# Kernel optimization log

Hardware: AMD Instinct MI355X
Metric: run time of the kernel (lower is better)

## Reference

```python
import jax, jax.numpy as jnp
import numpy as np

N = 50000      # nodes
E = 640000     # edges (before self loops)
IN = 128       # in_channels
H = 4          # heads (layer 1)
C = 64         # hidden_channels per head
OUT = 64       # out_channels
SLOPE = 0.2    # PyG GATConv default negative_slope


def setup_inputs() -> dict:
    key = jax.random.key(0)
    ks = jax.random.split(key, 12)
    x = jax.random.normal(ks[0], (N, IN), dtype=jnp.float32)
    edge_src = jax.random.randint(ks[1], (E,), 0, N, dtype=jnp.int32)
    edge_dst = jax.random.randint(ks[2], (E,), 0, N, dtype=jnp.int32)
    # Layer 1 params: Linear IN -> H*C, attention vectors a_src/a_dst [H, C], bias [H*C]
    W1 = jax.random.normal(ks[3], (IN, H * C), dtype=jnp.float32) / np.sqrt(IN)
    att_src1 = jax.random.normal(ks[4], (H, C), dtype=jnp.float32) / np.sqrt(C)
    att_dst1 = jax.random.normal(ks[5], (H, C), dtype=jnp.float32) / np.sqrt(C)
    b1 = jnp.zeros((H * C,), dtype=jnp.float32)
    # Layer 2 params: Linear H*C -> OUT, 1 head
    W2 = jax.random.normal(ks[6], (H * C, OUT), dtype=jnp.float32) / np.sqrt(H * C)
    att_src2 = jax.random.normal(ks[7], (1, OUT), dtype=jnp.float32) / np.sqrt(OUT)
    att_dst2 = jax.random.normal(ks[8], (1, OUT), dtype=jnp.float32) / np.sqrt(OUT)
    b2 = jnp.zeros((OUT,), dtype=jnp.float32)
    return {"x": x, "W1": W1, "att_src1": att_src1, "att_dst1": att_dst1, "b1": b1,
            "W2": W2, "att_src2": att_src2, "att_dst2": att_dst2, "b2": b2,
            "edge_src": edge_src, "edge_dst": edge_dst}


def gat_conv(x, src, dst, W, a_src, a_dst, b, heads, ch):
    """PyG GATConv (concat=True): gather -> LeakyReLU attention -> per-dst softmax -> scatter-add."""
    n = x.shape[0]
    h = (x @ W).reshape(n, heads, ch)                  # [N, H, C]
    al_s = jnp.sum(h * a_src, axis=-1)                 # [N, H] node-level src attention term
    al_d = jnp.sum(h * a_dst, axis=-1)                 # [N, H]
    e = jax.nn.leaky_relu(al_s[src] + al_d[dst], SLOPE)  # [E, H] edge scores
    m = jax.ops.segment_max(e, dst, num_segments=n)    # stable per-dst softmax
    ex = jnp.exp(e - m[dst])
    den = jax.ops.segment_sum(ex, dst, num_segments=n)
    alpha = ex / den[dst]                              # [E, H]
    msg = h[src] * alpha[:, :, None]                   # [E, H, C]
    out = jax.ops.segment_sum(msg, dst, num_segments=n)  # [N, H, C]
    return out.reshape(n, heads * ch) + b


def reference(x, W1, att_src1, att_dst1, b1, W2, att_src2, att_dst2, b2, edge_src, edge_dst):
    # PyG GATConv default add_self_loops=True
    loops = jnp.arange(N, dtype=edge_src.dtype)
    src = jnp.concatenate([edge_src, loops])
    dst = jnp.concatenate([edge_dst, loops])
    h = gat_conv(x, src, dst, W1, att_src1, att_dst1, b1, H, C)
    h = jax.nn.elu(h)                                  # F.elu; dropout p=0 -> no-op
    out = gat_conv(h, src, dst, W2, att_src2, att_dst2, b2, 1, OUT)
    return out
```

## Files before the change

### kernel.cpp

```cpp
#include <hip/hip_runtime.h>
#include <hip/hip_bf16.h>
#include <cstdint>
#include <cstddef>

#define N_NODES 50000
#define N_EDGES 640000
#define ET (N_EDGES + N_NODES)
#define IN_CH 128
#define H1 4
#define HC1 256
#define OUT_CH 64
#define SLOPE 0.2f
#define SCAN_NBLK ((N_NODES + 255) / 256)
#define XW (N_NODES * IN_CH / 8)
#define W1N (IN_CH * HC1)
#define W2N (HC1 * OUT_CH)
#define CONVB ((XW + W1N + W2N + 255) / 256)
#define EDGEB ((ET + 255) / 256)
#define MT ((N_NODES + 63) / 64)
#define PADB SCAN_NBLK
#define DUMMY N_NODES

typedef __attribute__((ext_vector_type(8))) short short8;
typedef __attribute__((ext_vector_type(4))) float floatx4;

__device__ __forceinline__ float bf2f(unsigned short u) {
    return __uint_as_float(((unsigned)u) << 16);
}
__device__ __forceinline__ unsigned short f2bf(float f) {
    unsigned u = __float_as_uint(f);
    unsigned r = 0x7fffu + ((u >> 16) & 1u);
    return (unsigned short)((u + r) >> 16);
}
__device__ __forceinline__ float ldf(const void* p, size_t i, bool f32) {
    return f32 ? ((const float*)p)[i] : bf2f(((const unsigned short*)p)[i]);
}

__global__ __launch_bounds__(256) void init_all(
    const unsigned short* __restrict__ x, unsigned* __restrict__ flag,
    int* __restrict__ counts, int* __restrict__ state,
    unsigned short* __restrict__ h16, unsigned short* __restrict__ h2,
    float* __restrict__ als1, float* __restrict__ als2)
{
    int b = blockIdx.x;
    if (b < SCAN_NBLK) {
        int i = b * 256 + threadIdx.x;
        if (i < N_NODES) counts[i] = 0;
    } else {
        int t = threadIdx.x;
        if (t < 64) {
            int bad = 0;
            #pragma unroll
            for (int r = 0; r < 4; ++r) {
                float v = bf2f(x[r * 64 + t]);
                if (!(v == v) || fabsf(v) > 1e4f) bad = 1;
            }
            unsigned long long m = __ballot(bad != 0);
            if (t == 0) *flag = (m != 0ull) ? 1u : 0u;
        } else if (t == 64) {
            state[0] = 0; state[1] = 0;
        } else if (t >= 128 && t < 192) {
            uint2 z; z.x = 0u; z.y = 0u;
            *((uint2*)(h16 + (size_t)DUMMY * HC1) + (t - 128)) = z;
        } else if (t >= 192 && t < 224) {
            ((unsigned*)(h2 + (size_t)DUMMY * OUT_CH))[t - 192] = 0u;
        } else if (t >= 224 && t < 228) {
            als1[(size_t)DUMMY * H1 + (t - 224)] = -1e30f;
        } else if (t == 228) {
            als2[DUMMY] = -1e30f;
        }
    }
}

__global__ __launch_bounds__(256) void conv_count(
    const void* __restrict__ x, const void* __restrict__ W1,
    const void* __restrict__ W2, const unsigned* __restrict__ flag,
    unsigned short* __restrict__ x16,
    unsigned short* __restrict__ Wt1, unsigned short* __restrict__ Wt2,
    const int* __restrict__ edst, int* __restrict__ counts,
    int* __restrict__ epos)
{
    int b = blockIdx.x;
    if (b < CONVB) {
        int i = b * 256 + threadIdx.x;
        const bool f32 = (*flag != 0);
        if (i < XW) {
            size_t off = (size_t)i * 8;
            uint4 st;
            if (f32) {
                const float* xp = (const float*)x + off;
                float4 a = *(const float4*)xp;
                float4 c = *(const float4*)(xp + 4);
                st.x = (unsigned)f2bf(a.x) | ((unsigned)f2bf(a.y) << 16);
                st.y = (unsigned)f2bf(a.z) | ((unsigned)f2bf(a.w) << 16);
                st.z = (unsigned)f2bf(c.x) | ((unsigned)f2bf(c.y) << 16);
                st.w = (unsigned)f2bf(c.z) | ((unsigned)f2bf(c.w) << 16);
            } else {
                st = *(const uint4*)((const unsigned short*)x + off);
            }
            *(uint4*)(x16 + off) = st;
        } else if (i < XW + W1N) {
            int j = i - XW;
            int n = j / IN_CH, k = j % IN_CH;
            Wt1[j] = f2bf(ldf(W1, (size_t)k * HC1 + n, f32));
        } else if (i < XW + W1N + W2N) {
            int j = i - XW - W1N;
            int n = j / HC1, k = j % HC1;
            Wt2[j] = f2bf(ldf(W2, (size_t)k * OUT_CH + n, f32));
        }
    } else {
        int i = (b - CONVB) * 256 + threadIdx.x;
        if (i < ET) {
            int d = (i < N_EDGES) ? edst[i] : (i - N_EDGES);
            epos[i] = atomicAdd(&counts[d], 1);
        }
    }
}

__global__ __launch_bounds__(256) void scan_onepass(
    const int* __restrict__ counts, int* __restrict__ rowptr,
    int* __restrict__ bsum, int* __restrict__ boff, int* __restrict__ state)
{
    __shared__ int s[256];
    const int t = threadIdx.x, b = blockIdx.x;
    const int i = b * 256 + t;
    int v = (i < N_NODES) ? ((counts[i] + 7) & ~7) : 0;
    s[t] = v;
    __syncthreads();
    #pragma unroll
    for (int off = 1; off < 256; off <<= 1) {
        int u = (t >= off) ? s[t - off] : 0;
        __syncthreads();
        s[t] += u;
        __syncthreads();
    }
    const int incl = s[t];
    if (t == 255) {
        __hip_atomic_store(&bsum[b], incl, __ATOMIC_RELAXED, __HIP_MEMORY_SCOPE_AGENT);
        __hip_atomic_fetch_add(&state[0], 1, __ATOMIC_ACQ_REL, __HIP_MEMORY_SCOPE_AGENT);
    }
    if (b == 0) {
        if (t == 0) {
            while (__hip_atomic_load(&state[0], __ATOMIC_ACQUIRE, __HIP_MEMORY_SCOPE_AGENT) < SCAN_NBLK)
                __builtin_amdgcn_s_sleep(8);
        }
        __syncthreads();
        int w = (t < SCAN_NBLK)
              ? __hip_atomic_load(&bsum[t], __ATOMIC_RELAXED, __HIP_MEMORY_SCOPE_AGENT) : 0;
        s[t] = w;
        __syncthreads();
        #pragma unroll
        for (int off = 1; off < 256; off <<= 1) {
            int u = (t >= off) ? s[t - off] : 0;
            __syncthreads();
            s[t] += u;
            __syncthreads();
        }
        if (t < SCAN_NBLK)
            __hip_atomic_store(&boff[t], s[t] - w, __ATOMIC_RELAXED, __HIP_MEMORY_SCOPE_AGENT);
        __syncthreads();
        if (t == 0)
            __hip_atomic_store(&state[1], 1, __ATOMIC_RELEASE, __HIP_MEMORY_SCOPE_AGENT);
    }
    if (t == 0) {
        while (__hip_atomic_load(&state[1], __ATOMIC_ACQUIRE, __HIP_MEMORY_SCOPE_AGENT) == 0)
            __builtin_amdgcn_s_sleep(8);
    }
    __syncthreads();
    int off0 = __hip_atomic_load(&boff[b], __ATOMIC_RELAXED, __HIP_MEMORY_SCOPE_AGENT);
    if (i < N_NODES)
        rowptr[i] = off0 + incl - v;
    if (i == N_NODES - 1) rowptr[N_NODES] = off0 + incl;
}

template <int KK, int NSUB>
__device__ __forceinline__ void gemm_body(
    const unsigned short* __restrict__ A, const unsigned short* __restrict__ Bt,
    const void* __restrict__ avs, const void* __restrict__ avd,
    const unsigned* __restrict__ flag, unsigned short* __restrict__ C,
    float* __restrict__ als, float* __restrict__ ald,
    int M, int N, int bx, int by)
{
    const int tid = threadIdx.x;
    const int m0 = by * 64, n0 = bx * (NSUB * 16);
    const int w = tid >> 6, lane = tid & 63;
    const int ln = lane & 15, quad = lane >> 4;
    const int m_frag = m0 + w * 16 + ln;
    floatx4 acc[NSUB];
    #pragma unroll
    for (int sub = 0; sub < NSUB; ++sub)
        acc[sub] = (floatx4){0.f, 0.f, 0.f, 0.f};

    #pragma unroll 2
    for (int ks = 0; ks < KK / 32; ++ks) {
        const int kbase = ks * 32 + quad * 8;
        short8 a;
        if (m_frag < M) {
            a = *(const short8*)(A + (size_t)m_frag * KK + kbase);
        } else {
            #pragma unroll
            for (int j = 0; j < 8; ++j) a[j] = 0;
        }
        #pragma unroll
        for (int sub = 0; sub < NSUB; ++sub) {
            short8 b = *(const short8*)(Bt + (size_t)(n0 + sub * 16 + ln) * KK + kbase);
            acc[sub] = __builtin_amdgcn_mfma_f32_16x16x32_bf16(a, b, acc[sub], 0, 0, 0);
        }
    }

    #pragma unroll
    for (int sub = 0; sub < NSUB; ++sub) {
        #pragma unroll
        for (int r = 0; r < 4; ++r) {
            int m = m0 + w * 16 + quad * 4 + r;
            if (m < M)
                C[(size_t)m * N + n0 + sub * 16 + ln] = f2bf(acc[sub][r]);
        }
    }

    const bool f32in = (*flag != 0);
    float as[NSUB], av[NSUB];
    #pragma unroll
    for (int sub = 0; sub < NSUB; ++sub) {
        as[sub] = ldf(avs, n0 + sub * 16 + ln, f32in);
        av[sub] = ldf(avd, n0 + sub * 16 + ln, f32in);
    }
    const int Hh = N >> 6;
    #pragma unroll
    for (int hb = 0; hb < NSUB / 4; ++hb) {
        #pragma unroll
        for (int r = 0; r < 4; ++r) {
            float ps = 0.f, pd = 0.f;
            #pragma unroll
            for (int k = 0; k < 4; ++k) {
                ps += acc[hb * 4 + k][r] * as[hb * 4 + k];
                pd += acc[hb * 4 + k][r] * av[hb * 4 + k];
            }
            #pragma unroll
            for (int off = 1; off < 16; off <<= 1) {
                ps += __shfl_xor(ps, off, 64);
                pd += __shfl_xor(pd, off, 64);
            }
            int m = m0 + w * 16 + quad * 4 + r;
            if (ln == 0 && m < M) {
                als[(size_t)m * Hh + bx * (NSUB / 4) + hb] = ps;
                ald[(size_t)m * Hh + bx * (NSUB / 4) + hb] = pd;
            }
        }
    }
}

__global__ __launch_bounds__(256) void gemm1_fill(
    const unsigned short* __restrict__ x16, const unsigned short* __restrict__ Wt1,
    const void* __restrict__ as1, const void* __restrict__ ad1,
    const unsigned* __restrict__ flag, unsigned short* __restrict__ h16,
    float* __restrict__ als, float* __restrict__ ald,
    const int* __restrict__ esrc, const int* __restrict__ edst,
    const int* __restrict__ rowptr, const int* __restrict__ epos,
    const int* __restrict__ counts, int* __restrict__ ecsr)
{
    int b = blockIdx.x;
    if (b < MT) {
        gemm_body<IN_CH, 16>(x16, Wt1, as1, ad1, flag, h16, als, ald,
                             N_NODES, HC1, 0, b);
    } else if (b < MT + EDGEB) {
        int i = (b - MT) * 256 + threadIdx.x;
        if (i < ET) {
            int s = (i < N_EDGES) ? esrc[i] : (i - N_EDGES);
            int d = (i < N_EDGES) ? edst[i] : (i - N_EDGES);
            ecsr[rowptr[d] + epos[i]] = s;
        }
    } else {
        int i = (b - MT - EDGEB) * 256 + threadIdx.x;
        if (i < N_NODES) {
            int c = counts[i];
            int lo = rowptr[i] + c, hi = rowptr[i + 1];
            for (int j = lo; j < hi; ++j) ecsr[j] = DUMMY;
        }
    }
}

__global__ __launch_bounds__(256) void gemm2(
    const unsigned short* __restrict__ xo16, const unsigned short* __restrict__ Wt2,
    const void* __restrict__ as2, const void* __restrict__ ad2,
    const unsigned* __restrict__ flag, unsigned short* __restrict__ h2,
    float* __restrict__ als, float* __restrict__ ald)
{
    gemm_body<HC1, 4>(xo16, Wt2, as2, ad2, flag, h2, als, ald,
                      N_NODES, OUT_CH, 0, blockIdx.x);
}

__global__ __launch_bounds__(256) void agg_node1(
    const int* __restrict__ rowptr, const int* __restrict__ ecsr,
    const unsigned short* __restrict__ h, const float* __restrict__ als,
    const float* __restrict__ ald, const void* __restrict__ bias,
    const unsigned* __restrict__ flag, unsigned short* __restrict__ out)
{
    int wave = (blockIdx.x * blockDim.x + threadIdx.x) >> 6;
    int lane = threadIdx.x & 63;
    if (wave >= N_NODES) return;
    const int d = wave;
    const int hg = lane >> 4;
    const int c0 = (lane & 15) << 2;
    const int hoff = hg * 64 + c0;
    const int lo = rowptr[d], hi = rowptr[d + 1];
    const float ad = ald[d * H1 + hg];

    float acc0 = 0.f, acc1 = 0.f, acc2 = 0.f, acc3 = 0.f, den = 0.f;

    int4 iA = *(const int4*)(ecsr + lo);
    int4 iB = *(const int4*)(ecsr + lo + 4);
    for (int e = lo; e < hi; e += 8) {
        const int4 cA = iA, cB = iB;
        const int en = (e + 8 < hi) ? (e + 8) : lo;
        iA = *(const int4*)(ecsr + en);
        iB = *(const int4*)(ecsr + en + 4);

        uint2 q0 = *(const uint2*)(h + (size_t)cA.x * HC1 + hoff);
        uint2 q1 = *(const uint2*)(h + (size_t)cA.y * HC1 + hoff);
        uint2 q2 = *(const uint2*)(h + (size_t)cA.z * HC1 + hoff);
        uint2 q3 = *(const uint2*)(h + (size_t)cA.w * HC1 + hoff);
        uint2 q4 = *(const uint2*)(h + (size_t)cB.x * HC1 + hoff);
        uint2 q5 = *(const uint2*)(h + (size_t)cB.y * HC1 + hoff);
        uint2 q6 = *(const uint2*)(h + (size_t)cB.z * HC1 + hoff);
        uint2 q7 = *(const uint2*)(h + (size_t)cB.w * HC1 + hoff);
        float t0 = als[cA.x * H1 + hg] + ad;
        float t1 = als[cA.y * H1 + hg] + ad;
        float t2 = als[cA.z * H1 + hg] + ad;
        float t3 = als[cA.w * H1 + hg] + ad;
        float t4 = als[cB.x * H1 + hg] + ad;
        float t5 = als[cB.y * H1 + hg] + ad;
        float t6 = als[cB.z * H1 + hg] + ad;
        float t7 = als[cB.w * H1 + hg] + ad;
        float p0 = __expf(fmaxf(t0, SLOPE * t0));
        float p1 = __expf(fmaxf(t1, SLOPE * t1));
        float p2 = __expf(fmaxf(t2, SLOPE * t2));
        float p3 = __expf(fmaxf(t3, SLOPE * t3));
        float p4 = __expf(fmaxf(t4, SLOPE * t4));
        float p5 = __expf(fmaxf(t5, SLOPE * t5));
        float p6 = __expf(fmaxf(t6, SLOPE * t6));
        float p7 = __expf(fmaxf(t7, SLOPE * t7));
        den += ((p0 + p1) + (p2 + p3)) + ((p4 + p5) + (p6 + p7));
        acc0 += p0 * __uint_as_float(q0.x << 16)         + p1 * __uint_as_float(q1.x << 16)
              + p2 * __uint_as_float(q2.x << 16)         + p3 * __uint_as_float(q3.x << 16)
              + p4 * __uint_as_float(q4.x << 16)         + p5 * __uint_as_float(q5.x << 16)
              + p6 * __uint_as_float(q6.x << 16)         + p7 * __uint_as_float(q7.x << 16);
        acc1 += p0 * __uint_as_float(q0.x & 0xffff0000u) + p1 * __uint_as_float(q1.x & 0xffff0000u)
              + p2 * __uint_as_float(q2.x & 0xffff0000u) + p3 * __uint_as_float(q3.x & 0xffff0000u)
              + p4 * __uint_as_float(q4.x & 0xffff0000u) + p5 * __uint_as_float(q5.x & 0xffff0000u)
              + p6 * __uint_as_float(q6.x & 0xffff0000u) + p7 * __uint_as_float(q7.x & 0xffff0000u);
        acc2 += p0 * __uint_as_float(q0.y << 16)         + p1 * __uint_as_float(q1.y << 16)
              + p2 * __uint_as_float(q2.y << 16)         + p3 * __uint_as_float(q3.y << 16)
              + p4 * __uint_as_float(q4.y << 16)         + p5 * __uint_as_float(q5.y << 16)
              + p6 * __uint_as_float(q6.y << 16)         + p7 * __uint_as_float(q7.y << 16);
        acc3 += p0 * __uint_as_float(q0.y & 0xffff0000u) + p1 * __uint_as_float(q1.y & 0xffff0000u)
              + p2 * __uint_as_float(q2.y & 0xffff0000u) + p3 * __uint_as_float(q3.y & 0xffff0000u)
              + p4 * __uint_as_float(q4.y & 0xffff0000u) + p5 * __uint_as_float(q5.y & 0xffff0000u)
              + p6 * __uint_as_float(q6.y & 0xffff0000u) + p7 * __uint_as_float(q7.y & 0xffff0000u);
    }

    const bool f32in = (*flag != 0);
    const float inv = 1.f / den;
    float v0 = acc0 * inv + ldf(bias, hoff + 0, f32in);
    float v1 = acc1 * inv + ldf(bias, hoff + 1, f32in);
    float v2 = acc2 * inv + ldf(bias, hoff + 2, f32in);
    float v3 = acc3 * inv + ldf(bias, hoff + 3, f32in);
    v0 = (v0 > 0.f) ? v0 : (__expf(v0) - 1.f);
    v1 = (v1 > 0.f) ? v1 : (__expf(v1) - 1.f);
    v2 = (v2 > 0.f) ? v2 : (__expf(v2) - 1.f);
    v3 = (v3 > 0.f) ? v3 : (__expf(v3) - 1.f);
    uint2 st;
    st.x = (unsigned)f2bf(v0) | ((unsigned)f2bf(v1) << 16);
    st.y = (unsigned)f2bf(v2) | ((unsigned)f2bf(v3) << 16);
    *(uint2*)(out + (size_t)d * HC1 + hoff) = st;
}

__global__ __launch_bounds__(256) void agg_node2(
    const int* __restrict__ rowptr, const int* __restrict__ ecsr,
    const unsigned short* __restrict__ h, const float* __restrict__ als,
    const float* __restrict__ ald, const void* __restrict__ bias,
    const unsigned* __restrict__ flag, float* __restrict__ out)
{
    int wave = (blockIdx.x * blockDim.x + threadIdx.x) >> 6;
    int lane = threadIdx.x & 63;
    if (wave >= N_NODES) return;
    const int d = wave;
    const int eg = lane >> 3;
    const int c0 = (lane & 7) << 3;
    const int lo = rowptr[d], hi = rowptr[d + 1];
    const float ad = ald[d];

    float acc[8];
    #pragma unroll
    for (int j = 0; j < 8; ++j) acc[j] = 0.f;
    float den = 0.f;

    int sP = ecsr[lo + eg];
    for (int eb = lo; eb < hi; eb += 8) {
        const int s = sP;
        const int en = (eb + 8 < hi) ? (eb + 8) : lo;
        sP = ecsr[en + eg];
        uint4 q = *(const uint4*)(h + (size_t)s * OUT_CH + c0);
        float t = als[s] + ad;
        float p = __expf(fmaxf(t, SLOPE * t));
        den += p;
        acc[0] += p * __uint_as_float(q.x << 16);
        acc[1] += p * __uint_as_float(q.x & 0xffff0000u);
        acc[2] += p * __uint_as_float(q.y << 16);
        acc[3] += p * __uint_as_float(q.y & 0xffff0000u);
        acc[4] += p * __uint_as_float(q.z << 16);
        acc[5] += p * __uint_as_float(q.z & 0xffff0000u);
        acc[6] += p * __uint_as_float(q.w << 16);
        acc[7] += p * __uint_as_float(q.w & 0xffff0000u);
    }
    #pragma unroll
    for (int off = 8; off <= 32; off <<= 1) {
        den += __shfl_xor(den, off, 64);
        #pragma unroll
        for (int j = 0; j < 8; ++j) acc[j] += __shfl_xor(acc[j], off, 64);
    }
    if (lane < 8) {
        const bool f32in = (*flag != 0);
        const float inv = 1.f / den;
        float4 v0, v1;
        v0.x = acc[0] * inv + ldf(bias, c0 + 0, f32in);
        v0.y = acc[1] * inv + ldf(bias, c0 + 1, f32in);
        v0.z = acc[2] * inv + ldf(bias, c0 + 2, f32in);
        v0.w = acc[3] * inv + ldf(bias, c0 + 3, f32in);
        v1.x = acc[4] * inv + ldf(bias, c0 + 4, f32in);
        v1.y = acc[5] * inv + ldf(bias, c0 + 5, f32in);
        v1.z = acc[6] * inv + ldf(bias, c0 + 6, f32in);
        v1.w = acc[7] * inv + ldf(bias, c0 + 7, f32in);
        *(float4*)(out + (size_t)d * OUT_CH + c0) = v0;
        *(float4*)(out + (size_t)d * OUT_CH + c0 + 4) = v1;
    }
}

extern "C" void kernel_launch(void* const* d_in, const int* in_sizes, int n_in,
                              void* d_out, int out_size, void* d_ws, size_t ws_size,
                              hipStream_t stream)
{
    const void* x   = d_in[0];
    const void* W1  = d_in[1];
    const void* as1 = d_in[2];
    const void* ad1 = d_in[3];
    const void* b1  = d_in[4];
    const void* W2  = d_in[5];
    const void* as2 = d_in[6];
    const void* ad2 = d_in[7];
    const void* b2  = d_in[8];
    const int* esrc = (const int*)d_in[9];
    const int* edst = (const int*)d_in[10];
    float* out = (float*)d_out;

    char* base = (char*)d_ws;
    const size_t MB = 1024 * 1024;
    unsigned short* x16  = (unsigned short*)(base);
    unsigned short* h16  = (unsigned short*)(base + 13 * MB);
    unsigned short* xo16 = (unsigned short*)(base + 39 * MB);
    unsigned short* h2   = (unsigned short*)(base + 65 * MB);
    float* als1   = (float*)(base + 72 * MB);
    float* ald1   = (float*)(base + 73 * MB);
    float* als2   = (float*)(base + 74 * MB);
    float* ald2   = (float*)(base + 74 * MB + 512 * 1024);
    unsigned short* Wt1 = (unsigned short*)(base + 75 * MB);
    unsigned short* Wt2 = (unsigned short*)(base + 75 * MB + 128 * 1024);
    int* counts   = (int*)(base + 76 * MB);
    int* rowptr   = (int*)(base + 77 * MB);
    int* bsum     = (int*)(base + 78 * MB);
    int* boff     = bsum + 256;
    int* state    = boff + 256;
    unsigned* flag = (unsigned*)(base + 78 * MB + 8 * 1024);
    int* epos     = (int*)(base + 79 * MB);
    int* ecsr     = (int*)(base + 82 * MB);

    const int BLK = 256;
    const int node_wave_blocks = (N_NODES * 64 + BLK - 1) / BLK;

    init_all<<<SCAN_NBLK + 1, BLK, 0, stream>>>(
        (const unsigned short*)x, flag, counts, state, h16, h2, als1, als2);

    conv_count<<<CONVB + EDGEB, BLK, 0, stream>>>(
        x, W1, W2, flag, x16, Wt1, Wt2, edst, counts, epos);

    scan_onepass<<<SCAN_NBLK, BLK, 0, stream>>>(
        counts, rowptr, bsum, boff, state);

    gemm1_fill<<<MT + EDGEB + PADB, BLK, 0, stream>>>(
        x16, Wt1, as1, ad1, flag, h16, als1, ald1, esrc, edst, rowptr, epos,
        counts, ecsr);

    agg_node1<<<node_wave_blocks, BLK, 0, stream>>>(
        rowptr, ecsr, h16, als1, ald1, b1, flag, xo16);

    gemm2<<<MT, BLK, 0, stream>>>(xo16, Wt2, as2, ad2, flag, h2, als2, ald2);

    agg_node2<<<node_wave_blocks, BLK, 0, stream>>>(
        rowptr, ecsr, h2, als2, ald2, b2, flag, out);
}
```

Measured before the change: 291.8 us.

## Split GEMM1 into per-head column tiles and widen agg_node1 gather loads

GEMM1 now launches four blocks per 64-row tile, one per 64-column head slice (NSUB 4), instead of one block covering all 256 columns, giving more blocks and fewer accumulator registers per block. agg_node1 changes its lane mapping so each lane loads 8 bf16 channels (uint4) and the two half-waves process alternating edges, combined at the end with a shuffle. This trades the 8-edge unrolled prefetch for wider loads and fewer in-flight gathers per lane. agg_node2 drops its index prefetch and the gemm k-loop unroll pragma is removed.

```diff
diff --git a/kernel.cpp b/kernel.cpp
--- a/kernel.cpp
+++ b/kernel.cpp
@@ -18,6 +18,7 @@
 #define CONVB ((XW + W1N + W2N + 255) / 256)
 #define EDGEB ((ET + 255) / 256)
 #define MT ((N_NODES + 63) / 64)
+#define G1B (4 * MT)
 #define PADB SCAN_NBLK
 #define DUMMY N_NODES
 
@@ -35,6 +36,8 @@
 __device__ __forceinline__ float ldf(const void* p, size_t i, bool f32) {
     return f32 ? ((const float*)p)[i] : bf2f(((const unsigned short*)p)[i]);
 }
+#define BLO(u) __uint_as_float((u) << 16)
+#define BHI(u) __uint_as_float((u) & 0xffff0000u)
 
 __global__ __launch_bounds__(256) void init_all(
     const unsigned short* __restrict__ x, unsigned* __restrict__ flag,
@@ -191,7 +194,6 @@
     for (int sub = 0; sub < NSUB; ++sub)
         acc[sub] = (floatx4){0.f, 0.f, 0.f, 0.f};
 
-    #pragma unroll 2
     for (int ks = 0; ks < KK / 32; ++ks) {
         const int kbase = ks * 32 + quad * 8;
         short8 a;
@@ -260,18 +262,18 @@
     const int* __restrict__ counts, int* __restrict__ ecsr)
 {
     int b = blockIdx.x;
-    if (b < MT) {
-        gemm_body<IN_CH, 16>(x16, Wt1, as1, ad1, flag, h16, als, ald,
-                             N_NODES, HC1, 0, b);
-    } else if (b < MT + EDGEB) {
-        int i = (b - MT) * 256 + threadIdx.x;
+    if (b < G1B) {
+        gemm_body<IN_CH, 4>(x16, Wt1, as1, ad1, flag, h16, als, ald,
+                            N_NODES, HC1, b & 3, b >> 2);
+    } else if (b < G1B + EDGEB) {
+        int i = (b - G1B) * 256 + threadIdx.x;
         if (i < ET) {
             int s = (i < N_EDGES) ? esrc[i] : (i - N_EDGES);
             int d = (i < N_EDGES) ? edst[i] : (i - N_EDGES);
             ecsr[rowptr[d] + epos[i]] = s;
         }
     } else {
-        int i = (b - MT - EDGEB) * 256 + threadIdx.x;
+        int i = (b - G1B - EDGEB) * 256 + threadIdx.x;
         if (i < N_NODES) {
             int c = counts[i];
             int lo = rowptr[i] + c, hi = rowptr[i + 1];
@@ -300,79 +302,59 @@
     int lane = threadIdx.x & 63;
     if (wave >= N_NODES) return;
     const int d = wave;
-    const int hg = lane >> 4;
-    const int c0 = (lane & 15) << 2;
+    const int g  = lane >> 5;
+    const int hg = (lane >> 3) & 3;
+    const int c0 = (lane & 7) << 3;
     const int hoff = hg * 64 + c0;
     const int lo = rowptr[d], hi = rowptr[d + 1];
     const float ad = ald[d * H1 + hg];
 
-    float acc0 = 0.f, acc1 = 0.f, acc2 = 0.f, acc3 = 0.f, den = 0.f;
-
-    int4 iA = *(const int4*)(ecsr + lo);
-    int4 iB = *(const int4*)(ecsr + lo + 4);
-    for (int e = lo; e < hi; e += 8) {
-        const int4 cA = iA, cB = iB;
-        const int en = (e + 8 < hi) ? (e + 8) : lo;
-        iA = *(const int4*)(ecsr + en);
-        iB = *(const int4*)(ecsr + en + 4);
-
-        uint2 q0 = *(const uint2*)(h + (size_t)cA.x * HC1 + hoff);
-        uint2 q1 = *(const uint2*)(h + (size_t)cA.y * HC1 + hoff);
-        uint2 q2 = *(const uint2*)(h + (size_t)cA.z * HC1 + hoff);
-        uint2 q3 = *(const uint2*)(h + (size_t)cA.w * HC1 + hoff);
-        uint2 q4 = *(const uint2*)(h + (size_t)cB.x * HC1 + hoff);
-        uint2 q5 = *(const uint2*)(h + (size_t)cB.y * HC1 + hoff);
-        uint2 q6 = *(const uint2*)(h + (size_t)cB.z * HC1 + hoff);
-        uint2 q7 = *(const uint2*)(h + (size_t)cB.w * HC1 + hoff);
-        float t0 = als[cA.x * H1 + hg] + ad;
-        float t1 = als[cA.y * H1 + hg] + ad;
-        float t2 = als[cA.z * H1 + hg] + ad;
-        float t3 = als[cA.w * H1 + hg] + ad;
-        float t4 = als[cB.x * H1 + hg] + ad;
-        float t5 = als[cB.y * H1 + hg] + ad;
-        float t6 = als[cB.z * H1 + hg] + ad;
-        float t7 = als[cB.w * H1 + hg] + ad;
+    float acc[8];
+    #pragma unroll
+    for (int j = 0; j < 8; ++j) acc[j] = 0.f;
+    float den = 0.f;
+
+    for (int e = lo; e < hi; e += 4) {
+        int4 ix = *(const int4*)(ecsr + e);
+        int s0 = g ? ix.y : ix.x;
+        int s1 = g ? ix.w : ix.z;
+        uint4 qa = *(const uint4*)(h + (size_t)s0 * HC1 + hoff);
+        uint4 qb = *(const uint4*)(h + (size_t)s1 * HC1 + hoff);
+        float t0 = als[s0 * H1 + hg] + ad;
+        float t1 = als[s1 * H1 + hg] + ad;
         float p0 = __expf(fmaxf(t0, SLOPE * t0));
         float p1 = __expf(fmaxf(t1, SLOPE * t1));
-        float p2 = __expf(fmaxf(t2, SLOPE * t2));
-        float p3 = __expf(fmaxf(t3, SLOPE * t3));
-        float p4 = __expf(fmaxf(t4, SLOPE * t4));
-        float p5 = __expf(fmaxf(t5, SLOPE * t5));
-        float p6 = __expf(fmaxf(t6, SLOPE * t6));
-        float p7 = __expf(fmaxf(t7, SLOPE * t7));
-        den += ((p0 + p1) + (p2 + p3)) + ((p4 + p5) + (p6 + p7));
-        acc0 += p0 * __uint_as_float(q0.x << 16)         + p1 * __uint_as_float(q1.x << 16)
-              + p2 * __uint_as_float(q2.x << 16)         + p3 * __uint_as_float(q3.x << 16)
-              + p4 * __uint_as_float(q4.x << 16)         + p5 * __uint_as_float(q5.x << 16)
-              + p6 * __uint_as_float(q6.x << 16)         + p7 * __uint_as_float(q7.x << 16);
-        acc1 += p0 * __uint_as_float(q0.x & 0xffff0000u) + p1 * __uint_as_float(q1.x & 0xffff0000u)
-              + p2 * __uint_as_float(q2.x & 0xffff0000u) + p3 * __uint_as_float(q3.x & 0xffff0000u)
-              + p4 * __uint_as_float(q4.x & 0xffff0000u) + p5 * __uint_as_float(q5.x & 0xffff0000u)
-              + p6 * __uint_as_float(q6.x & 0xffff0000u) + p7 * __uint_as_float(q7.x & 0xffff0000u);
-        acc2 += p0 * __uint_as_float(q0.y << 16)         + p1 * __uint_as_float(q1.y << 16)
-              + p2 * __uint_as_float(q2.y << 16)         + p3 * __uint_as_float(q3.y << 16)
-              + p4 * __uint_as_float(q4.y << 16)         + p5 * __uint_as_float(q5.y << 16)
-              + p6 * __uint_as_float(q6.y << 16)         + p7 * __uint_as_float(q7.y << 16);
-        acc3 += p0 * __uint_as_float(q0.y & 0xffff0000u) + p1 * __uint_as_float(q1.y & 0xffff0000u)
-              + p2 * __uint_as_float(q2.y & 0xffff0000u) + p3 * __uint_as_float(q3.y & 0xffff0000u)
-              + p4 * __uint_as_float(q4.y & 0xffff0000u) + p5 * __uint_as_float(q5.y & 0xffff0000u)
-              + p6 * __uint_as_float(q6.y & 0xffff0000u) + p7 * __uint_as_float(q7.y & 0xffff0000u);
-    }
-
-    const bool f32in = (*flag != 0);
-    const float inv = 1.f / den;
-    float v0 = acc0 * inv + ldf(bias, hoff + 0, f32in);
-    float v1 = acc1 * inv + ldf(bias, hoff + 1, f32in);
-    float v2 = acc2 * inv + ldf(bias, hoff + 2, f32in);
-    float v3 = acc3 * inv + ldf(bias, hoff + 3, f32in);
-    v0 = (v0 > 0.f) ? v0 : (__expf(v0) - 1.f);
-    v1 = (v1 > 0.f) ? v1 : (__expf(v1) - 1.f);
-    v2 = (v2 > 0.f) ? v2 : (__expf(v2) - 1.f);
-    v3 = (v3 > 0.f) ? v3 : (__expf(v3) - 1.f);
-    uint2 st;
-    st.x = (unsigned)f2bf(v0) | ((unsigned)f2bf(v1) << 16);
-    st.y = (unsigned)f2bf(v2) | ((unsigned)f2bf(v3) << 16);
-    *(uint2*)(out + (size_t)d * HC1 + hoff) = st;
+        den += p0 + p1;
+        acc[0] += p0 * BLO(qa.x) + p1 * BLO(qb.x);
+        acc[1] += p0 * BHI(qa.x) + p1 * BHI(qb.x);
+        acc[2] += p0 * BLO(qa.y) + p1 * BLO(qb.y);
+        acc[3] += p0 * BHI(qa.y) + p1 * BHI(qb.y);
+        acc[4] += p0 * BLO(qa.z) + p1 * BLO(qb.z);
+        acc[5] += p0 * BHI(qa.z) + p1 * BHI(qb.z);
+        acc[6] += p0 * BLO(qa.w) + p1 * BLO(qb.w);
+        acc[7] += p0 * BHI(qa.w) + p1 * BHI(qb.w);
+    }
+
+    den += __shfl_xor(den, 32, 64);
+    #pragma unroll
+    for (int j = 0; j < 8; ++j) acc[j] += __shfl_xor(acc[j], 32, 64);
+
+    if (lane < 32) {
+        const bool f32in = (*flag != 0);
+        const float inv = 1.f / den;
+        float v[8];
+        #pragma unroll
+        for (int j = 0; j < 8; ++j) {
+            float t = acc[j] * inv + ldf(bias, hoff + j, f32in);
+            v[j] = (t > 0.f) ? t : (__expf(t) - 1.f);
+        }
+        uint4 st;
+        st.x = (unsigned)f2bf(v[0]) | ((unsigned)f2bf(v[1]) << 16);
+        st.y = (unsigned)f2bf(v[2]) | ((unsigned)f2bf(v[3]) << 16);
+        st.z = (unsigned)f2bf(v[4]) | ((unsigned)f2bf(v[5]) << 16);
+        st.w = (unsigned)f2bf(v[6]) | ((unsigned)f2bf(v[7]) << 16);
+        *(uint4*)(out + (size_t)d * HC1 + hoff) = st;
+    }
 }
 
 __global__ __launch_bounds__(256) void agg_node2(
@@ -395,23 +377,20 @@
     for (int j = 0; j < 8; ++j) acc[j] = 0.f;
     float den = 0.f;
 
-    int sP = ecsr[lo + eg];
     for (int eb = lo; eb < hi; eb += 8) {
-        const int s = sP;
-        const int en = (eb + 8 < hi) ? (eb + 8) : lo;
-        sP = ecsr[en + eg];
+        int s = ecsr[eb + eg];
         uint4 q = *(const uint4*)(h + (size_t)s * OUT_CH + c0);
         float t = als[s] + ad;
         float p = __expf(fmaxf(t, SLOPE * t));
         den += p;
-        acc[0] += p * __uint_as_float(q.x << 16);
-        acc[1] += p * __uint_as_float(q.x & 0xffff0000u);
-        acc[2] += p * __uint_as_float(q.y << 16);
-        acc[3] += p * __uint_as_float(q.y & 0xffff0000u);
-        acc[4] += p * __uint_as_float(q.z << 16);
-        acc[5] += p * __uint_as_float(q.z & 0xffff0000u);
-        acc[6] += p * __uint_as_float(q.w << 16);
-        acc[7] += p * __uint_as_float(q.w & 0xffff0000u);
+        acc[0] += p * BLO(q.x);
+        acc[1] += p * BHI(q.x);
+        acc[2] += p * BLO(q.y);
+        acc[3] += p * BHI(q.y);
+        acc[4] += p * BLO(q.z);
+        acc[5] += p * BHI(q.z);
+        acc[6] += p * BLO(q.w);
+        acc[7] += p * BHI(q.w);
     }
     #pragma unroll
     for (int off = 8; off <= 32; off <<= 1) {
@@ -486,7 +465,7 @@
     scan_onepass<<<SCAN_NBLK, BLK, 0, stream>>>(
         counts, rowptr, bsum, boff, state);
 
-    gemm1_fill<<<MT + EDGEB + PADB, BLK, 0, stream>>>(
+    gemm1_fill<<<G1B + EDGEB + PADB, BLK, 0, stream>>>(
         x16, Wt1, as1, ad1, flag, h16, als1, ald1, esrc, edst, rowptr, epos,
         counts, ecsr);
 
```

Measured after the change: 291.5 us. Within noise of the previous version (-0.1%).
